# Kernel optimization log

Hardware: AMD Instinct MI355X
Metric: run time of the kernel (lower is better)

Reference implementation:

```python
import jax, jax.numpy as jnp
import numpy as np

DIM = 96          # channels (= groups for depthwise conv)
NUM_EXPERTS = 6
TOP_K = 3
B, H, W = 8, 192, 192


def _dwconv(x, w, b):
    # depthwise 3x3, stride 1, pad 1, groups = DIM (flag == 'C' branch)
    y = jax.lax.conv_general_dilated(
        x, w, window_strides=(1, 1), padding=((1, 1), (1, 1)),
        feature_group_count=DIM,
        dimension_numbers=('NCHW', 'OIHW', 'NCHW'))
    return y + b[None, :, None, None]


def _expert(x, w1, b1, w2, b2):
    return _dwconv(jax.nn.relu(_dwconv(x, w1, b1)), w2, b2)


def _gate(x, w_fc0, b_fc0, w_fc1, b_fc1):
    # AdaptiveMaxPool2d(1) + AdaptiveAvgPool2d(1), then flatten -> (B, DIM)
    pooled = jnp.max(x, axis=(2, 3)) + jnp.mean(x, axis=(2, 3))
    g = jax.nn.leaky_relu(pooled @ w_fc1.T + b_fc1, negative_slope=0.2)
    noise = jax.nn.softplus(pooled @ w_fc0.T + b_fc0)
    mu = jnp.mean(noise, axis=1, keepdims=True)
    sd = jnp.std(noise, axis=1, keepdims=True, ddof=1)  # torch.std is unbiased
    scores = g + (noise - mu) / sd
    _, idx = jax.lax.top_k(scores, TOP_K)  # (B, K)
    mask = jnp.any(jax.nn.one_hot(idx, NUM_EXPERTS, dtype=jnp.float32) > 0, axis=1)  # (B, E)
    # non-top-k logits of g set to -inf, softmax over experts
    return jax.nn.softmax(jnp.where(mask, g, -jnp.inf), axis=1)


def setup_inputs() -> dict:
    key = jax.random.key(0)
    ks = jax.random.split(key, 9)
    s = 0.05
    return {
        'x': jax.random.normal(ks[0], (B, DIM, H, W), jnp.float32),
        'w_fc0': jax.random.normal(ks[1], (NUM_EXPERTS, DIM), jnp.float32) * s,
        'b_fc0': jax.random.normal(ks[2], (NUM_EXPERTS,), jnp.float32) * s,
        'w_fc1': jax.random.normal(ks[3], (NUM_EXPERTS, DIM), jnp.float32) * s,
        'b_fc1': jax.random.normal(ks[4], (NUM_EXPERTS,), jnp.float32) * s,
        'ew1': jax.random.normal(ks[5], (NUM_EXPERTS, DIM, 1, 3, 3), jnp.float32) * s,
        'eb1': jax.random.normal(ks[6], (NUM_EXPERTS, DIM), jnp.float32) * s,
        'ew2': jax.random.normal(ks[7], (NUM_EXPERTS, DIM, 1, 3, 3), jnp.float32) * s,
        'eb2': jax.random.normal(ks[8], (NUM_EXPERTS, DIM), jnp.float32) * s,
    }


def reference(x, w_fc0, b_fc0, w_fc1, b_fc1, ew1, eb1, ew2, eb2):
    cof = _gate(x, w_fc0, b_fc0, w_fc1, b_fc1)  # (B, E), zero for non-top-k
    # Dense dispatch: experts with cof==0 contribute nothing, matching the
    # torch masked gather/scatter-accumulate loop exactly.
    outs = jax.vmap(lambda w1, b1, w2, b2: _expert(x, w1, b1, w2, b2))(
        ew1, eb1, ew2, eb2)  # (E, B, C, H, W)
    return jnp.einsum('ebchw,be->bchw', outs, cof)
```

## Files before the change

### kernel.cpp

```cpp
#include <hip/hip_runtime.h>
#include <math.h>

#define DIM 96
#define NE 6
#define NB 8
#define H 192
#define W 192
#define HW (H * W)
#define NQ 4
#define QF4 (HW / 4 / NQ)

__global__ __launch_bounds__(256) void pool_partial(const float* __restrict__ x,
                                                    float* __restrict__ pmax,
                                                    float* __restrict__ psum) {
    int bc = blockIdx.x;
    int q = blockIdx.y;
    const float4* xp = (const float4*)(x + (size_t)bc * HW) + q * QF4;
    int tid = threadIdx.x;
    float vmax = -INFINITY, vsum = 0.f;
    for (int i = tid; i < QF4; i += 256) {
        float4 v = xp[i];
        vmax = fmaxf(vmax, fmaxf(fmaxf(v.x, v.y), fmaxf(v.z, v.w)));
        vsum += v.x + v.y + v.z + v.w;
    }
    for (int off = 32; off; off >>= 1) {
        vmax = fmaxf(vmax, __shfl_down(vmax, off, 64));
        vsum += __shfl_down(vsum, off, 64);
    }
    __shared__ float smax[4], ssum[4];
    if ((tid & 63) == 0) { smax[tid >> 6] = vmax; ssum[tid >> 6] = vsum; }
    __syncthreads();
    if (tid == 0) {
        float m = smax[0], s = ssum[0];
        for (int w = 1; w < 4; ++w) { m = fmaxf(m, smax[w]); s += ssum[w]; }
        pmax[q * (NB * DIM) + bc] = m;
        psum[q * (NB * DIM) + bc] = s;
    }
}

__global__ __launch_bounds__(128) void gate_kernel(const float* __restrict__ pmax,
                                                   const float* __restrict__ psum,
                                                   const float* __restrict__ w_fc0,
                                                   const float* __restrict__ b_fc0,
                                                   const float* __restrict__ w_fc1,
                                                   const float* __restrict__ b_fc1,
                                                   float* __restrict__ cof) {
    __shared__ float sp[NB * DIM];
    __shared__ float sw1[NE * DIM], sw0[NE * DIM];
    __shared__ float z1s[NB * NE], z0s[NB * NE];
    int tid = threadIdx.x;
    for (int i = tid; i < NB * DIM; i += 128) {
        float m = pmax[i], s = psum[i];
        for (int q = 1; q < NQ; ++q) {
            m = fmaxf(m, pmax[q * (NB * DIM) + i]);
            s += psum[q * (NB * DIM) + i];
        }
        sp[i] = m + s * (1.0f / (float)HW);
    }
    for (int i = tid; i < NE * DIM; i += 128) {
        sw1[i] = w_fc1[i];
        sw0[i] = w_fc0[i];
    }
    __syncthreads();
    if (tid < 2 * NB * NE) {
        int pair = (tid < NB * NE) ? tid : tid - NB * NE;
        int b = pair / NE, e = pair - b * NE;
        const float* wp = ((tid < NB * NE) ? sw1 : sw0) + e * DIM;
        float z = (tid < NB * NE) ? b_fc1[e] : b_fc0[e];
        const float* pp = sp + b * DIM;
        for (int i = 0; i < DIM; ++i) z = fmaf(pp[i], wp[i], z);
        if (tid < NB * NE) z1s[pair] = z; else z0s[pair] = z;
    }
    __syncthreads();
    if (tid < NB) {
        int b = tid;
        float g[NE], noise[NE];
        for (int e = 0; e < NE; ++e) {
            float z1 = z1s[b * NE + e], z0 = z0s[b * NE + e];
            g[e] = (z1 > 0.f) ? z1 : 0.2f * z1;
            noise[e] = (z0 > 20.f) ? z0 : log1pf(expf(z0));
        }
        float mu = 0.f;
        for (int e = 0; e < NE; ++e) mu += noise[e];
        mu *= (1.0f / NE);
        float var = 0.f;
        for (int e = 0; e < NE; ++e) { float d = noise[e] - mu; var += d * d; }
        var *= (1.0f / (NE - 1));
        float sd = sqrtf(var);
        float scores[NE];
        for (int e = 0; e < NE; ++e) scores[e] = g[e] + (noise[e] - mu) / sd;
        bool chosen[NE] = {false, false, false, false, false, false};
        for (int k = 0; k < 3; ++k) {
            float best = -INFINITY; int bi = 0;
            for (int e = 0; e < NE; ++e)
                if (!chosen[e] && scores[e] > best) { best = scores[e]; bi = e; }
            chosen[bi] = true;
        }
        float m = -INFINITY;
        for (int e = 0; e < NE; ++e) if (chosen[e]) m = fmaxf(m, g[e]);
        float s = 0.f;
        for (int e = 0; e < NE; ++e) if (chosen[e]) s += expf(g[e] - m);
        float inv = 1.0f / s;
        for (int e = 0; e < NE; ++e)
            cof[b * NE + e] = chosen[e] ? expf(g[e] - m) * inv : 0.f;
    }
}

#define TX 64
#define TY 32
#define IX (TX + 4)
#define IY (TY + 4)
#define YX (TX + 2)
#define YY (TY + 2)

__global__ __launch_bounds__(256) void moe_kernel(const float* __restrict__ x,
                                                  const float* __restrict__ ew1,
                                                  const float* __restrict__ eb1,
                                                  const float* __restrict__ ew2,
                                                  const float* __restrict__ eb2,
                                                  const float* __restrict__ cof,
                                                  float* __restrict__ out) {
    __shared__ float xs[IY][IX];
    __shared__ float ys[YY][YX];
    const int tile = blockIdx.x;
    const int c = blockIdx.y;
    const int b = blockIdx.z;
    const int tx0 = (tile % (W / TX)) * TX;
    const int ty0 = (tile / (W / TX)) * TY;
    const int tid = threadIdx.x;
    const int tx = tid & 63;
    const int wv = (tid >> 6) & 3;

    const float* xp = x + ((size_t)(b * DIM + c)) * HW;

    #pragma unroll
    for (int rr = 0; rr < 9; ++rr) {
        int r = wv + rr * 4;
        int gh = ty0 + r - 2;
        int gw = tx0 + tx - 2;
        float v = 0.f, v2 = 0.f;
        if (gh >= 0 && gh < H) {
            if (gw >= 0 && gw < W) v = xp[gh * W + gw];
            int gw2 = gw + 64;
            if (tx < 4 && gw2 < W) v2 = xp[gh * W + gw2];
        }
        xs[r][tx] = v;
        if (tx < 4) xs[r][tx + 64] = v2;
    }

    const bool topB = (ty0 == 0), botB = (ty0 == H - TY);
    const bool leftB = (tx0 == 0), rightB = (tx0 == W - TX);
    const int zr0 = topB ? 0 : -1;
    const int zr1 = botB ? (YY - 1) : -1;
    const bool lzero = leftB && (tx == 0);

    float acc[8];
    #pragma unroll
    for (int i = 0; i < 8; ++i) acc[i] = 0.f;

    const int rs = wv * 8 + (wv ? 1 : 0);
    const int r2 = wv * 8;

    for (int e = 0; e < NE; ++e) {
        float ce = cof[b * NE + e];
        if (ce == 0.f) continue;
        const float* w1 = ew1 + (size_t)(e * DIM + c) * 9;
        const float* w2 = ew2 + (size_t)(e * DIM + c) * 9;
        float w1r[9], w2r[9];
        #pragma unroll
        for (int k = 0; k < 9; ++k) { w1r[k] = w1[k]; w2r[k] = w2[k]; }
        const float bb1 = eb1[e * DIM + c];
        const float bb2 = eb2[e * DIM + c];

        __syncthreads();

        {
            float a0 = xs[rs][tx], a1 = xs[rs][tx + 1], a2 = xs[rs][tx + 2];
            float b0 = xs[rs + 1][tx], b1 = xs[rs + 1][tx + 1], b2 = xs[rs + 1][tx + 2];
            #pragma unroll
            for (int j = 0; j < 9; ++j) {
                int r = rs + j;
                float c0 = xs[r + 2][tx], c1 = xs[r + 2][tx + 1], c2 = xs[r + 2][tx + 2];
                float s = fmaf(w1r[0], a0, fmaf(w1r[1], a1, fmaf(w1r[2], a2, bb1)));
                s = fmaf(w1r[3], b0, fmaf(w1r[4], b1, fmaf(w1r[5], b2, s)));
                s = fmaf(w1r[6], c0, fmaf(w1r[7], c1, fmaf(w1r[8], c2, s)));
                float v = fmaxf(s, 0.f);
                if (r == zr0 || r == zr1 || lzero) v = 0.f;
                ys[r][tx] = v;
                a0 = b0; a1 = b1; a2 = b2;
                b0 = c0; b1 = c1; b2 = c2;
            }
        }
        if (tid < 2 * YY) {
            int r = tid >> 1;
            int cc = 64 + (tid & 1);
            float s = bb1;
            #pragma unroll
            for (int dr = 0; dr < 3; ++dr)
                #pragma unroll
                for (int dc = 0; dc < 3; ++dc)
                    s = fmaf(w1r[dr * 3 + dc], xs[r + dr][cc + dc], s);
            float v = fmaxf(s, 0.f);
            if (r == zr0 || r == zr1 || (rightB && cc == YX - 1)) v = 0.f;
            ys[r][cc] = v;
        }
        __syncthreads();

        {
            float p0 = ys[r2][tx], p1 = ys[r2][tx + 1], p2 = ys[r2][tx + 2];
            float q0 = ys[r2 + 1][tx], q1 = ys[r2 + 1][tx + 1], q2 = ys[r2 + 1][tx + 2];
            #pragma unroll
            for (int j = 0; j < 8; ++j) {
                float u0 = ys[r2 + j + 2][tx], u1 = ys[r2 + j + 2][tx + 1], u2 = ys[r2 + j + 2][tx + 2];
                float s = fmaf(w2r[0], p0, fmaf(w2r[1], p1, fmaf(w2r[2], p2, bb2)));
                s = fmaf(w2r[3], q0, fmaf(w2r[4], q1, fmaf(w2r[5], q2, s)));
                s = fmaf(w2r[6], u0, fmaf(w2r[7], u1, fmaf(w2r[8], u2, s)));
                acc[j] = fmaf(ce, s, acc[j]);
                p0 = q0; p1 = q1; p2 = q2;
                q0 = u0; q1 = u1; q2 = u2;
            }
        }
    }

    float* op = out + ((size_t)(b * DIM + c)) * HW + (size_t)(ty0 + r2) * W + tx0 + tx;
    #pragma unroll
    for (int j = 0; j < 8; ++j) op[j * W] = acc[j];
}

extern "C" void kernel_launch(void* const* d_in, const int* in_sizes, int n_in,
                              void* d_out, int out_size, void* d_ws, size_t ws_size,
                              hipStream_t stream) {
    const float* x     = (const float*)d_in[0];
    const float* w_fc0 = (const float*)d_in[1];
    const float* b_fc0 = (const float*)d_in[2];
    const float* w_fc1 = (const float*)d_in[3];
    const float* b_fc1 = (const float*)d_in[4];
    const float* ew1   = (const float*)d_in[5];
    const float* eb1   = (const float*)d_in[6];
    const float* ew2   = (const float*)d_in[7];
    const float* eb2   = (const float*)d_in[8];
    float* out = (float*)d_out;

    float* pmax = (float*)d_ws;
    float* psum = pmax + NQ * NB * DIM;
    float* cof  = psum + NQ * NB * DIM;

    dim3 pg(NB * DIM, NQ);
    pool_partial<<<pg, 256, 0, stream>>>(x, pmax, psum);
    gate_kernel<<<1, 128, 0, stream>>>(pmax, psum, w_fc0, b_fc0, w_fc1, b_fc1, cof);
    dim3 grid((W / TX) * (H / TY), DIM, NB);
    moe_kernel<<<grid, 256, 0, stream>>>(x, ew1, eb1, ew2, eb2, cof, out);
}
```

Before: 280.1 us.

## Compute 2x4 output micro-tiles per thread with vectorized LDS reads

Each thread now computes a 2-row by 4-column block for both depthwise convolution stages instead of a column strip of one pixel per row. Shared-memory rows are read as float4/float2 windows, the ys tile stride is padded to 68 floats so rows stay float4-aligned, and the final output is written with float4 stores. The aim is to cut LDS instruction count and increase register reuse of neighbouring pixels. In exchange, the halo rows and columns now need separate handling paths across more threads, and float4 LDS access patterns may cause bank conflicts.

After: 309.6 us. +10.5%, slower.

```diff
diff --git a/kernel.cpp b/kernel.cpp
--- a/kernel.cpp
+++ b/kernel.cpp
@@ -108,10 +108,10 @@
 
 #define TX 64
 #define TY 32
-#define IX (TX + 4)
-#define IY (TY + 4)
-#define YX (TX + 2)
-#define YY (TY + 2)
+#define IX 68
+#define IY 36
+#define YSX 68
+#define YSY 34
 
 __global__ __launch_bounds__(256) void moe_kernel(const float* __restrict__ x,
                                                   const float* __restrict__ ew1,
@@ -121,7 +121,7 @@
                                                   const float* __restrict__ cof,
                                                   float* __restrict__ out) {
     __shared__ float xs[IY][IX];
-    __shared__ float ys[YY][YX];
+    __shared__ float ys[YSY][YSX];
     const int tile = blockIdx.x;
     const int c = blockIdx.y;
     const int b = blockIdx.z;
@@ -129,7 +129,9 @@
     const int ty0 = (tile / (W / TX)) * TY;
     const int tid = threadIdx.x;
     const int tx = tid & 63;
-    const int wv = (tid >> 6) & 3;
+    const int wv = tid >> 6;
+    const int q = tid & 15;
+    const int g = tid >> 4;
 
     const float* xp = x + ((size_t)(b * DIM + c)) * HW;
 
@@ -150,81 +152,118 @@
 
     const bool topB = (ty0 == 0), botB = (ty0 == H - TY);
     const bool leftB = (tx0 == 0), rightB = (tx0 == W - TX);
-    const int zr0 = topB ? 0 : -1;
-    const int zr1 = botB ? (YY - 1) : -1;
-    const bool lzero = leftB && (tx == 0);
-
-    float acc[8];
-    #pragma unroll
-    for (int i = 0; i < 8; ++i) acc[i] = 0.f;
-
-    const int rs = wv * 8 + (wv ? 1 : 0);
-    const int r2 = wv * 8;
+
+    float acc0[4] = {0.f, 0.f, 0.f, 0.f};
+    float acc1[4] = {0.f, 0.f, 0.f, 0.f};
 
     for (int e = 0; e < NE; ++e) {
         float ce = cof[b * NE + e];
         if (ce == 0.f) continue;
-        const float* w1 = ew1 + (size_t)(e * DIM + c) * 9;
-        const float* w2 = ew2 + (size_t)(e * DIM + c) * 9;
+        const float* w1p = ew1 + (size_t)(e * DIM + c) * 9;
+        const float* w2p = ew2 + (size_t)(e * DIM + c) * 9;
         float w1r[9], w2r[9];
         #pragma unroll
-        for (int k = 0; k < 9; ++k) { w1r[k] = w1[k]; w2r[k] = w2[k]; }
+        for (int k = 0; k < 9; ++k) { w1r[k] = w1p[k]; w2r[k] = w2p[k]; }
         const float bb1 = eb1[e * DIM + c];
         const float bb2 = eb2[e * DIM + c];
 
         __syncthreads();
 
         {
-            float a0 = xs[rs][tx], a1 = xs[rs][tx + 1], a2 = xs[rs][tx + 2];
-            float b0 = xs[rs + 1][tx], b1 = xs[rs + 1][tx + 1], b2 = xs[rs + 1][tx + 2];
-            #pragma unroll
-            for (int j = 0; j < 9; ++j) {
-                int r = rs + j;
-                float c0 = xs[r + 2][tx], c1 = xs[r + 2][tx + 1], c2 = xs[r + 2][tx + 2];
-                float s = fmaf(w1r[0], a0, fmaf(w1r[1], a1, fmaf(w1r[2], a2, bb1)));
-                s = fmaf(w1r[3], b0, fmaf(w1r[4], b1, fmaf(w1r[5], b2, s)));
-                s = fmaf(w1r[6], c0, fmaf(w1r[7], c1, fmaf(w1r[8], c2, s)));
-                float v = fmaxf(s, 0.f);
-                if (r == zr0 || r == zr1 || lzero) v = 0.f;
-                ys[r][tx] = v;
-                a0 = b0; a1 = b1; a2 = b2;
-                b0 = c0; b1 = c1; b2 = c2;
-            }
-        }
-        if (tid < 2 * YY) {
-            int r = tid >> 1;
-            int cc = 64 + (tid & 1);
+            const int R = 2 * g, C = 4 * q;
+            float win[4][6];
+            #pragma unroll
+            for (int r = 0; r < 4; ++r) {
+                float4 a = *(const float4*)&xs[R + r][C];
+                float2 p = *(const float2*)&xs[R + r][C + 4];
+                win[r][0] = a.x; win[r][1] = a.y; win[r][2] = a.z;
+                win[r][3] = a.w; win[r][4] = p.x; win[r][5] = p.y;
+            }
+            float o0[4], o1[4];
+            #pragma unroll
+            for (int j = 0; j < 4; ++j) {
+                float s0 = bb1, s1 = bb1;
+                #pragma unroll
+                for (int dr = 0; dr < 3; ++dr) {
+                    s0 = fmaf(w1r[dr * 3 + 0], win[dr][j],
+                         fmaf(w1r[dr * 3 + 1], win[dr][j + 1],
+                         fmaf(w1r[dr * 3 + 2], win[dr][j + 2], s0)));
+                    s1 = fmaf(w1r[dr * 3 + 0], win[dr + 1][j],
+                         fmaf(w1r[dr * 3 + 1], win[dr + 1][j + 1],
+                         fmaf(w1r[dr * 3 + 2], win[dr + 1][j + 2], s1)));
+                }
+                o0[j] = fmaxf(s0, 0.f);
+                o1[j] = fmaxf(s1, 0.f);
+            }
+            if (topB && g == 0) { o0[0] = o0[1] = o0[2] = o0[3] = 0.f; }
+            if (leftB && q == 0) { o0[0] = 0.f; o1[0] = 0.f; }
+            *(float4*)&ys[R][C]     = make_float4(o0[0], o0[1], o0[2], o0[3]);
+            *(float4*)&ys[R + 1][C] = make_float4(o1[0], o1[1], o1[2], o1[3]);
+        }
+        if (tid < 32) {
+            int r = 32 + (tid & 1);
+            int C = 4 * (tid >> 1);
+            float o[4];
+            #pragma unroll
+            for (int j = 0; j < 4; ++j) {
+                float s = bb1;
+                #pragma unroll
+                for (int dr = 0; dr < 3; ++dr)
+                    s = fmaf(w1r[dr * 3 + 0], xs[r + dr][C + j],
+                        fmaf(w1r[dr * 3 + 1], xs[r + dr][C + j + 1],
+                        fmaf(w1r[dr * 3 + 2], xs[r + dr][C + j + 2], s)));
+                o[j] = fmaxf(s, 0.f);
+            }
+            if (botB && r == 33) { o[0] = o[1] = o[2] = o[3] = 0.f; }
+            if (leftB && C == 0) o[0] = 0.f;
+            *(float4*)&ys[r][C] = make_float4(o[0], o[1], o[2], o[3]);
+        } else if (tid < 100) {
+            int t2 = tid - 32;
+            int cc = 64 + (t2 & 1);
+            int r = t2 >> 1;
             float s = bb1;
             #pragma unroll
             for (int dr = 0; dr < 3; ++dr)
+                s = fmaf(w1r[dr * 3 + 0], xs[r + dr][cc],
+                    fmaf(w1r[dr * 3 + 1], xs[r + dr][cc + 1],
+                    fmaf(w1r[dr * 3 + 2], xs[r + dr][cc + 2], s)));
+            float v = fmaxf(s, 0.f);
+            if ((topB && r == 0) || (botB && r == 33) || (rightB && cc == 65)) v = 0.f;
+            ys[r][cc] = v;
+        }
+        __syncthreads();
+
+        {
+            const int R = 2 * g, C = 4 * q;
+            float win[4][6];
+            #pragma unroll
+            for (int r = 0; r < 4; ++r) {
+                float4 a = *(const float4*)&ys[R + r][C];
+                float2 p = *(const float2*)&ys[R + r][C + 4];
+                win[r][0] = a.x; win[r][1] = a.y; win[r][2] = a.z;
+                win[r][3] = a.w; win[r][4] = p.x; win[r][5] = p.y;
+            }
+            #pragma unroll
+            for (int j = 0; j < 4; ++j) {
+                float s0 = bb2, s1 = bb2;
                 #pragma unroll
-                for (int dc = 0; dc < 3; ++dc)
-                    s = fmaf(w1r[dr * 3 + dc], xs[r + dr][cc + dc], s);
-            float v = fmaxf(s, 0.f);
-            if (r == zr0 || r == zr1 || (rightB && cc == YX - 1)) v = 0.f;
-            ys[r][cc] = v;
-        }
-        __syncthreads();
-
-        {
-            float p0 = ys[r2][tx], p1 = ys[r2][tx + 1], p2 = ys[r2][tx + 2];
-            float q0 = ys[r2 + 1][tx], q1 = ys[r2 + 1][tx + 1], q2 = ys[r2 + 1][tx + 2];
-            #pragma unroll
-            for (int j = 0; j < 8; ++j) {
-                float u0 = ys[r2 + j + 2][tx], u1 = ys[r2 + j + 2][tx + 1], u2 = ys[r2 + j + 2][tx + 2];
-                float s = fmaf(w2r[0], p0, fmaf(w2r[1], p1, fmaf(w2r[2], p2, bb2)));
-                s = fmaf(w2r[3], q0, fmaf(w2r[4], q1, fmaf(w2r[5], q2, s)));
-                s = fmaf(w2r[6], u0, fmaf(w2r[7], u1, fmaf(w2r[8], u2, s)));
-                acc[j] = fmaf(ce, s, acc[j]);
-                p0 = q0; p1 = q1; p2 = q2;
-                q0 = u0; q1 = u1; q2 = u2;
-            }
-        }
-    }
-
-    float* op = out + ((size_t)(b * DIM + c)) * HW + (size_t)(ty0 + r2) * W + tx0 + tx;
-    #pragma unroll
-    for (int j = 0; j < 8; ++j) op[j * W] = acc[j];
+                for (int dr = 0; dr < 3; ++dr) {
+                    s0 = fmaf(w2r[dr * 3 + 0], win[dr][j],
+                         fmaf(w2r[dr * 3 + 1], win[dr][j + 1],
+                         fmaf(w2r[dr * 3 + 2], win[dr][j + 2], s0)));
+                    s1 = fmaf(w2r[dr * 3 + 0], win[dr + 1][j],
+                         fmaf(w2r[dr * 3 + 1], win[dr + 1][j + 1],
+                         fmaf(w2r[dr * 3 + 2], win[dr + 1][j + 2], s1)));
+                }
+                acc0[j] = fmaf(ce, s0, acc0[j]);
+                acc1[j] = fmaf(ce, s1, acc1[j]);
+            }
+        }
+    }
+
+    float* op = out + ((size_t)(b * DIM + c)) * HW + (size_t)(ty0 + 2 * g) * W + tx0 + 4 * q;
+    *(float4*)op       = make_float4(acc0[0], acc0[1], acc0[2], acc0[3]);
+    *(float4*)(op + W) = make_float4(acc1[0], acc1[1], acc1[2], acc1[3]);
 }
 
 extern "C" void kernel_launch(void* const* d_in, const int* in_sizes, int n_in,
```
